# Performance work log

Hardware: AMD Instinct MI355X
Metric: run time of the kernel (lower is better)

The kernel has to match this reference:

```python
import jax, jax.numpy as jnp
import numpy as np

ALPHA = 0.2  # leaky relu slope


def setup_inputs() -> dict:
    key = jax.random.key(0)
    k_h, k_adj, k_w, k_a = jax.random.split(key, 4)
    B, N, F_in, F_out, H = 4, 2048, 128, 64, 4
    h = jax.random.normal(k_h, (B, N, F_in), dtype=jnp.float32)
    adj = jax.random.randint(k_adj, (N, N), 0, 2).astype(jnp.float32)
    # xavier_uniform with gain=1.414 (as in reset_parameters)
    gain = 1.414
    lim_w = gain * np.sqrt(6.0 / (F_in + F_out))
    W = jax.random.uniform(k_w, (H, F_in, F_out), minval=-lim_w, maxval=lim_w, dtype=jnp.float32)
    lim_a = gain * np.sqrt(6.0 / (2 * F_out + 1))
    a = jax.random.uniform(k_a, (H, 2 * F_out, 1), minval=-lim_a, maxval=lim_a, dtype=jnp.float32)
    return {"h": h, "adj": adj, "W": W, "a": a}


def reference(h, adj, W, a):
    B, N, _ = h.shape
    F_out = W.shape[2]
    # per-head linear transform: [B, N, H, F_out]
    ht = jnp.einsum('hio,bni->bnho', W, h)
    # split attention vector into src/dst halves; a^T [h_i; h_j] = a_src.h_i + a_dst.h_j
    a_src = a[:, :F_out, 0]   # [H, F_out]
    a_dst = a[:, F_out:, 0]   # [H, F_out]
    e_src = jnp.einsum('bnho,ho->bnh', ht, a_src)  # score contribution of node i (rows)
    e_dst = jnp.einsum('bnho,ho->bnh', ht, a_dst)  # score contribution of node j (cols)
    e = e_src[:, :, None, :] + e_dst[:, None, :, :]           # [B, N, N, H]
    e = jnp.where(e >= 0, e, ALPHA * e)                        # leaky relu
    e = e + (-1e20 * (1.0 - adj))[None, :, :, None]            # adjacency mask (shared over batch/heads)
    att = jax.nn.softmax(e, axis=2)                            # softmax over neighbors j
    # dropout p=0.0 (eval-mode reference): identity
    h_prime = jnp.einsum('bmnh,bnho->bmho', att, ht)           # [B, N, H, F_out]
    return h_prime.reshape(B, N, -1)                           # concat heads -> [B, N, H*F_out]
```

## Files before the change

kernel.cpp:

```cpp
#include <hip/hip_runtime.h>

#define ALPHA 0.2f
#define LOG2E 1.44269504088896340736f

constexpr int BB  = 4;
constexpr int NN  = 2048;
constexpr int FIN = 128;
constexpr int FO  = 64;
constexpr int HH  = 4;
constexpr int CC  = BB * HH;

using half8   = __attribute__((ext_vector_type(8))) _Float16;
using floatx4 = __attribute__((ext_vector_type(4))) float;

__device__ __forceinline__ float fast_exp2(float x) {
#if __has_builtin(__builtin_amdgcn_exp2f)
  return __builtin_amdgcn_exp2f(x);
#else
  return exp2f(x);
#endif
}

union PK4 { _Float16 f[4]; uint2 u; };

__global__ __launch_bounds__(256) void gat_k1_prep(
    const float* __restrict__ h, const float* __restrict__ W,
    const float* __restrict__ a, _Float16* __restrict__ htT,
    float* __restrict__ esrcT, float* __restrict__ edst) {
  const int blk = blockIdx.x;
  const int c  = blk >> 5;
  const int n0 = (blk & 31) * 64;
  const int b = c >> 2, hh = c & 3;
  const int t = threadIdx.x;
  const int w = t >> 6, lane = t & 63;
  const int q = lane >> 4, r16 = lane & 15;

  __shared__ __align__(16) _Float16 Xs[64 * 128];
  __shared__ __align__(16) _Float16 WT[64 * 128];
  __shared__ float wasb[128];
  __shared__ float wadb[128];

  {
    const int k = t & 127;
    const float* wrow = W + ((size_t)hh * 128 + k) * 64;
    const float* av = a + hh * 128 + ((t >> 7) << 6);
    float s = 0.f;
#pragma unroll
    for (int o = 0; o < 16; ++o) {
      const float4 wv = *(const float4*)(wrow + o * 4);
      const float4 av4 = *(const float4*)(av + o * 4);
      s += wv.x * av4.x + wv.y * av4.y + wv.z * av4.z + wv.w * av4.w;
    }
    if (t < 128) wasb[k] = s; else wadb[k] = s;
  }

  {
    const int k = t >> 1, fh = (t & 1) * 32;
    const float* wsrc = W + ((size_t)hh * 128 + k) * 64 + fh;
    const int chunk = k >> 3, within = k & 7;
#pragma unroll
    for (int i = 0; i < 8; ++i) {
      const float4 v = *(const float4*)(wsrc + i * 4);
      const _Float16 f4[4] = {(_Float16)v.x, (_Float16)v.y,
                              (_Float16)v.z, (_Float16)v.w};
#pragma unroll
      for (int u = 0; u < 4; ++u) {
        const int f = fh + i * 4 + u;
        WT[f * 128 + ((chunk ^ (f & 15)) << 3) + within] = f4[u];
      }
    }
  }

  __syncthreads();

  {
    const int r = t >> 2, cq = t & 3;
    const float* hsrc = h + ((size_t)(b * NN + n0 + r)) * FIN + cq * 32;
    float es = 0.f, ed = 0.f;
#pragma unroll
    for (int i = 0; i < 8; ++i) {
      const float4 v = *(const float4*)(hsrc + i * 4);
      const float4 ws = *(const float4*)&wasb[cq * 32 + i * 4];
      const float4 wd = *(const float4*)&wadb[cq * 32 + i * 4];
      es += v.x * ws.x + v.y * ws.y + v.z * ws.z + v.w * ws.w;
      ed += v.x * wd.x + v.y * wd.y + v.z * wd.z + v.w * wd.w;
      PK4 pk;
      pk.f[0] = (_Float16)v.x; pk.f[1] = (_Float16)v.y;
      pk.f[2] = (_Float16)v.z; pk.f[3] = (_Float16)v.w;
      const int chunk = cq * 4 + (i >> 1);
      *(uint2*)&Xs[r * 128 + ((chunk ^ (r & 15)) << 3) + (i & 1) * 4] = pk.u;
    }
    es += __shfl_xor(es, 1, 64); es += __shfl_xor(es, 2, 64);
    ed += __shfl_xor(ed, 1, 64); ed += __shfl_xor(ed, 2, 64);
    if (cq == 0) {
      esrcT[(size_t)(n0 + r) * CC + c] = es * LOG2E;
      edst[(size_t)c * NN + n0 + r]    = ed * LOG2E;
    }
  }

  __syncthreads();

  floatx4 acc[4];
#pragma unroll
  for (int ft = 0; ft < 4; ++ft) acc[ft] = floatx4{0.f, 0.f, 0.f, 0.f};

  half8 afrag[4];
#pragma unroll
  for (int ks = 0; ks < 4; ++ks) {
    const int slot = (ks * 4 + q) ^ r16;
    afrag[ks] = *(const half8*)&Xs[(w * 16 + r16) * 128 + (slot << 3)];
  }
#pragma unroll
  for (int ks = 0; ks < 4; ++ks) {
#pragma unroll
    for (int ft = 0; ft < 4; ++ft) {
      const int fr = ft * 16 + r16;
      const int slot = (ks * 4 + q) ^ (fr & 15);
      const half8 bfrag = *(const half8*)&WT[fr * 128 + (slot << 3)];
      acc[ft] = __builtin_amdgcn_mfma_f32_16x16x32_f16(afrag[ks], bfrag,
                                                       acc[ft], 0, 0, 0);
    }
  }

#pragma unroll
  for (int ft = 0; ft < 4; ++ft) {
    PK4 pk;
#pragma unroll
    for (int x = 0; x < 4; ++x) pk.f[x] = (_Float16)acc[ft][x];
    const int fcol = ft * 16 + r16;
    const int n = n0 + w * 16 + q * 4;
    *(uint2*)(htT + ((size_t)c * FO + fcol) * NN + n) = pk.u;
  }
}

__global__ __launch_bounds__(256) void gat_k2_stats(
    const float* __restrict__ adj, const float* __restrict__ esrcT,
    const float* __restrict__ edst, unsigned* __restrict__ adjbits,
    float* __restrict__ rmaxT) {
  const int t = threadIdx.x;
  const int w = t >> 6, l = t & 63;
  const int m = blockIdx.x * 4 + w;

  __shared__ float eds[16 * 520];

  float areg[32];
  const float* arow = adj + (size_t)m * NN;
#pragma unroll
  for (int j = 0; j < 32; ++j) areg[j] = arow[j * 64 + l];

#pragma unroll
  for (int j = 0; j < 32; ++j) {
    const unsigned long long mask = __ballot(areg[j] != 0.f);
    if (l == 0) {
      adjbits[m * 64 + j * 2 + 0] = (unsigned)mask;
      adjbits[m * 64 + j * 2 + 1] = (unsigned)(mask >> 32);
    }
  }

  float4 mv[4];
#pragma unroll
  for (int i = 0; i < 4; ++i) mv[i] = float4{-3.0e38f, -3.0e38f, -3.0e38f, -3.0e38f};

  for (int ch = 0; ch < 4; ++ch) {
    __syncthreads();
    {
#pragma unroll
      for (int i = 0; i < 8; ++i) {
        const int idx = t + i * 256;
        const int cc = idx >> 7, nf = idx & 127;
        const float4 v =
            *(const float4*)(edst + (size_t)cc * NN + ch * 512 + nf * 4);
        *(float4*)&eds[cc * 520 + nf * 4] = v;
      }
    }
    __syncthreads();
#pragma unroll
    for (int j2 = 0; j2 < 8; ++j2) {
      const bool on = (areg[ch * 8 + j2] != 0.f);
      const int nl = j2 * 64 + l;
#pragma unroll
      for (int i = 0; i < 4; ++i) {
        float4 e4;
        e4.x = eds[(i * 4 + 0) * 520 + nl];
        e4.y = eds[(i * 4 + 1) * 520 + nl];
        e4.z = eds[(i * 4 + 2) * 520 + nl];
        e4.w = eds[(i * 4 + 3) * 520 + nl];
        mv[i].x = fmaxf(mv[i].x, on ? e4.x : -3.0e38f);
        mv[i].y = fmaxf(mv[i].y, on ? e4.y : -3.0e38f);
        mv[i].z = fmaxf(mv[i].z, on ? e4.z : -3.0e38f);
        mv[i].w = fmaxf(mv[i].w, on ? e4.w : -3.0e38f);
      }
    }
  }

#pragma unroll
  for (int off = 1; off < 64; off <<= 1) {
#pragma unroll
    for (int i = 0; i < 4; ++i) {
      mv[i].x = fmaxf(mv[i].x, __shfl_xor(mv[i].x, off, 64));
      mv[i].y = fmaxf(mv[i].y, __shfl_xor(mv[i].y, off, 64));
      mv[i].z = fmaxf(mv[i].z, __shfl_xor(mv[i].z, off, 64));
      mv[i].w = fmaxf(mv[i].w, __shfl_xor(mv[i].w, off, 64));
    }
  }
  if (l == 0) {
#pragma unroll
    for (int i = 0; i < 4; ++i) {
      const float4 es = *(const float4*)&esrcT[(size_t)m * CC + i * 4];
      float4 o;
      const float sx = es.x + mv[i].x; o.x = (sx >= 0.f) ? sx : ALPHA * sx;
      const float sy = es.y + mv[i].y; o.y = (sy >= 0.f) ? sy : ALPHA * sy;
      const float sz = es.z + mv[i].z; o.z = (sz >= 0.f) ? sz : ALPHA * sz;
      const float sw = es.w + mv[i].w; o.w = (sw >= 0.f) ? sw : ALPHA * sw;
      *(float4*)&rmaxT[(size_t)m * CC + i * 4] = o;
    }
  }
}

__global__ __launch_bounds__(1024) void gat_k3_pv(
    const _Float16* __restrict__ htT, const float* __restrict__ esrcT,
    const float* __restrict__ edst, const unsigned* __restrict__ adjbits,
    const float* __restrict__ rmaxT, float* __restrict__ out) {
  const int blk = blockIdx.x;
  const int c = blk >> 5;
  const int m0 = (blk & 31) * 64;
  const int b = c >> 2, hh = c & 3;
  const int t = threadIdx.x;
  const int w = t >> 6;
  const int kg = w >> 2;
  const int wl = w & 3;
  const int lane = t & 63;
  const int q = lane >> 4, r16 = lane & 15;
  const int row = m0 + wl * 16 + r16;

  __shared__ __align__(16) char smem[64512];
  _Float16* Vt = (_Float16*)smem;
  float* abuf = (float*)smem;

  const float em = esrcT[(size_t)row * CC + c];
  const float rm = rmaxT[(size_t)row * CC + c];
  const float em1 = em - rm;
  const float em2 = fmaf(ALPHA, em, -rm);
  const float* edc = edst + (size_t)c * NN;
  const unsigned* abrow = adjbits + (size_t)row * 64;
  const _Float16* vsrc = htT + (size_t)c * FO * NN;

  const int f0 = t >> 4, sg0 = t & 15;
  const size_t goff0 = (size_t)f0 * NN + (size_t)((sg0 ^ (f0 & 15)) * 8);

  floatx4 acc[4];
#pragma unroll
  for (int ft = 0; ft < 4; ++ft) acc[ft] = floatx4{0.f, 0.f, 0.f, 0.f};
  floatx4 accs = floatx4{0.f, 0.f, 0.f, 0.f};

  half8 ones;
#pragma unroll
  for (int k = 0; k < 8; ++k) ones[k] = (_Float16)1.0f;

#define STAGE(BUF, NBASE)                                                      \
  __builtin_amdgcn_global_load_lds(                                            \
      (const __attribute__((address_space(1))) void*)(vsrc + goff0 + (NBASE)), \
      (__attribute__((address_space(3))) void*)(smem + (BUF)*16384 + t*16),    \
      16, 0, 0)

  STAGE(0, 0);

  for (int step = 0; step < 16; ++step) {
    const int n0k = step * 128 + kg * 32;
    half8 afrag;
    const unsigned bits = abrow[step * 4 + kg] >> (q * 8);
    const float4 ea = *(const float4*)(edc + n0k + q * 8);
    const float4 eb = *(const float4*)(edc + n0k + q * 8 + 4);
    const float xs[8] = {ea.x, ea.y, ea.z, ea.w, eb.x, eb.y, eb.z, eb.w};
#pragma unroll
    for (int k = 0; k < 8; ++k) {
      const float t1 = em1 + xs[k];
      const float t2 = fmaf(ALPHA, xs[k], em2);
      float tt = fmaxf(t1, t2);
      tt = ((bits >> k) & 1u) ? tt : -3.0e38f;
      afrag[k] = (_Float16)fast_exp2(tt);
    }
    __syncthreads();
    if (step + 1 < 16) STAGE((step + 1) & 1, (step + 1) * 128);
    const int bufo = (step & 1) * 8192;
    accs = __builtin_amdgcn_mfma_f32_16x16x32_f16(afrag, ones, accs, 0, 0, 0);
#pragma unroll
    for (int ft = 0; ft < 4; ++ft) {
      const int fr = ft * 16 + r16;
      const int oct = kg * 4 + q;
      const half8 bfrag =
          *(const half8*)&Vt[bufo + fr * 128 + ((oct ^ (fr & 15)) << 3)];
      acc[ft] = __builtin_amdgcn_mfma_f32_16x16x32_f16(afrag, bfrag,
                                                       acc[ft], 0, 0, 0);
    }
  }

  __syncthreads();
  if (kg >= 1) {
    const int base = ((kg - 1) * 256 + (t & 255)) * 21;
#pragma unroll
    for (int ft = 0; ft < 4; ++ft)
#pragma unroll
      for (int x = 0; x < 4; ++x) abuf[base + ft * 4 + x] = acc[ft][x];
#pragma unroll
    for (int x = 0; x < 4; ++x) abuf[base + 16 + x] = accs[x];
  }
  __syncthreads();
  if (kg == 0) {
#pragma unroll
    for (int g = 0; g < 3; ++g) {
      const int base = (g * 256 + t) * 21;
#pragma unroll
      for (int ft = 0; ft < 4; ++ft)
#pragma unroll
        for (int x = 0; x < 4; ++x) acc[ft][x] += abuf[base + ft * 4 + x];
#pragma unroll
      for (int x = 0; x < 4; ++x) accs[x] += abuf[base + 16 + x];
    }
#pragma unroll
    for (int x = 0; x < 4; ++x) {
      const float rinv = 1.0f / accs[x];
      const int mrow = m0 + wl * 16 + q * 4 + x;
      float* op = out + ((size_t)b * NN + mrow) * 256 + hh * 64;
#pragma unroll
      for (int ft = 0; ft < 4; ++ft) op[ft * 16 + r16] = acc[ft][x] * rinv;
    }
  }
#undef STAGE
}

extern "C" void kernel_launch(void* const* d_in, const int* in_sizes, int n_in,
                              void* d_out, int out_size, void* d_ws, size_t ws_size,
                              hipStream_t stream) {
  const float* h   = (const float*)d_in[0];
  const float* adj = (const float*)d_in[1];
  const float* W   = (const float*)d_in[2];
  const float* a   = (const float*)d_in[3];
  float* out = (float*)d_out;

  char* ws = (char*)d_ws;
  _Float16* htT   = (_Float16*)(ws);
  float* esrcT    = (float*)(ws + 4 * 1024 * 1024);
  float* edst     = (float*)(ws + 4 * 1024 * 1024 + 131072);
  unsigned* abits = (unsigned*)(ws + 4 * 1024 * 1024 + 2 * 131072);
  float* rmaxT    = (float*)(ws + 4 * 1024 * 1024 + 2 * 131072 + 524288);

  gat_k1_prep<<<dim3(CC * (NN / 64)), dim3(256), 0, stream>>>(h, W, a, htT, esrcT, edst);
  gat_k2_stats<<<dim3(NN / 4), dim3(256), 0, stream>>>(adj, esrcT, edst, abits, rmaxT);
  gat_k3_pv<<<dim3(CC * (NN / 64)), dim3(1024), 0, stream>>>(htT, esrcT, edst, abits, rmaxT, out);
}
```

Baseline: 128.4 us.

## Replace masked row max with global column max bound and fuse stats kernel

New measurement: 112.1 us. 1.15x faster.

```diff
diff --git a/kernel.cpp b/kernel.cpp
--- a/kernel.cpp
+++ b/kernel.cpp
@@ -23,22 +23,44 @@
 
 union PK4 { _Float16 f[4]; uint2 u; };
 
-__global__ __launch_bounds__(256) void gat_k1_prep(
+__global__ __launch_bounds__(256) void gat_k12(
     const float* __restrict__ h, const float* __restrict__ W,
-    const float* __restrict__ a, _Float16* __restrict__ htT,
-    float* __restrict__ esrcT, float* __restrict__ edst) {
+    const float* __restrict__ a, const float* __restrict__ adj,
+    _Float16* __restrict__ htT, float* __restrict__ esrcT,
+    float* __restrict__ edst, float* __restrict__ gpart,
+    unsigned* __restrict__ adjbits) {
   const int blk = blockIdx.x;
-  const int c  = blk >> 5;
-  const int n0 = (blk & 31) * 64;
-  const int b = c >> 2, hh = c & 3;
   const int t = threadIdx.x;
   const int w = t >> 6, lane = t & 63;
+
+  if (blk >= 512) {
+    const int m = (blk - 512) * 4 + w;
+    float areg[32];
+    const float* arow = adj + (size_t)m * NN;
+#pragma unroll
+    for (int j = 0; j < 32; ++j) areg[j] = arow[j * 64 + lane];
+#pragma unroll
+    for (int j = 0; j < 32; ++j) {
+      const unsigned long long mask = __ballot(areg[j] != 0.f);
+      if (lane == 0) {
+        adjbits[m * 64 + j * 2 + 0] = (unsigned)mask;
+        adjbits[m * 64 + j * 2 + 1] = (unsigned)(mask >> 32);
+      }
+    }
+    return;
+  }
+
+  const int c  = blk >> 5;
+  const int nt = blk & 31;
+  const int n0 = nt * 64;
+  const int b = c >> 2, hh = c & 3;
   const int q = lane >> 4, r16 = lane & 15;
 
   __shared__ __align__(16) _Float16 Xs[64 * 128];
   __shared__ __align__(16) _Float16 WT[64 * 128];
   __shared__ float wasb[128];
   __shared__ float wadb[128];
+  __shared__ float edsh[64];
 
   {
     const int k = t & 127;
@@ -93,12 +115,21 @@
     es += __shfl_xor(es, 1, 64); es += __shfl_xor(es, 2, 64);
     ed += __shfl_xor(ed, 1, 64); ed += __shfl_xor(ed, 2, 64);
     if (cq == 0) {
+      const float edl = ed * LOG2E;
       esrcT[(size_t)(n0 + r) * CC + c] = es * LOG2E;
-      edst[(size_t)c * NN + n0 + r]    = ed * LOG2E;
-    }
-  }
-
-  __syncthreads();
+      edst[(size_t)c * NN + n0 + r]    = edl;
+      edsh[r] = edl;
+    }
+  }
+
+  __syncthreads();
+
+  if (t < 64) {
+    float v = edsh[t];
+#pragma unroll
+    for (int off = 1; off < 64; off <<= 1) v = fmaxf(v, __shfl_xor(v, off, 64));
+    if (t == 0) gpart[c * 32 + nt] = v;
+  }
 
   floatx4 acc[4];
 #pragma unroll
@@ -133,94 +164,10 @@
   }
 }
 
-__global__ __launch_bounds__(256) void gat_k2_stats(
-    const float* __restrict__ adj, const float* __restrict__ esrcT,
-    const float* __restrict__ edst, unsigned* __restrict__ adjbits,
-    float* __restrict__ rmaxT) {
-  const int t = threadIdx.x;
-  const int w = t >> 6, l = t & 63;
-  const int m = blockIdx.x * 4 + w;
-
-  __shared__ float eds[16 * 520];
-
-  float areg[32];
-  const float* arow = adj + (size_t)m * NN;
-#pragma unroll
-  for (int j = 0; j < 32; ++j) areg[j] = arow[j * 64 + l];
-
-#pragma unroll
-  for (int j = 0; j < 32; ++j) {
-    const unsigned long long mask = __ballot(areg[j] != 0.f);
-    if (l == 0) {
-      adjbits[m * 64 + j * 2 + 0] = (unsigned)mask;
-      adjbits[m * 64 + j * 2 + 1] = (unsigned)(mask >> 32);
-    }
-  }
-
-  float4 mv[4];
-#pragma unroll
-  for (int i = 0; i < 4; ++i) mv[i] = float4{-3.0e38f, -3.0e38f, -3.0e38f, -3.0e38f};
-
-  for (int ch = 0; ch < 4; ++ch) {
-    __syncthreads();
-    {
-#pragma unroll
-      for (int i = 0; i < 8; ++i) {
-        const int idx = t + i * 256;
-        const int cc = idx >> 7, nf = idx & 127;
-        const float4 v =
-            *(const float4*)(edst + (size_t)cc * NN + ch * 512 + nf * 4);
-        *(float4*)&eds[cc * 520 + nf * 4] = v;
-      }
-    }
-    __syncthreads();
-#pragma unroll
-    for (int j2 = 0; j2 < 8; ++j2) {
-      const bool on = (areg[ch * 8 + j2] != 0.f);
-      const int nl = j2 * 64 + l;
-#pragma unroll
-      for (int i = 0; i < 4; ++i) {
-        float4 e4;
-        e4.x = eds[(i * 4 + 0) * 520 + nl];
-        e4.y = eds[(i * 4 + 1) * 520 + nl];
-        e4.z = eds[(i * 4 + 2) * 520 + nl];
-        e4.w = eds[(i * 4 + 3) * 520 + nl];
-        mv[i].x = fmaxf(mv[i].x, on ? e4.x : -3.0e38f);
-        mv[i].y = fmaxf(mv[i].y, on ? e4.y : -3.0e38f);
-        mv[i].z = fmaxf(mv[i].z, on ? e4.z : -3.0e38f);
-        mv[i].w = fmaxf(mv[i].w, on ? e4.w : -3.0e38f);
-      }
-    }
-  }
-
-#pragma unroll
-  for (int off = 1; off < 64; off <<= 1) {
-#pragma unroll
-    for (int i = 0; i < 4; ++i) {
-      mv[i].x = fmaxf(mv[i].x, __shfl_xor(mv[i].x, off, 64));
-      mv[i].y = fmaxf(mv[i].y, __shfl_xor(mv[i].y, off, 64));
-      mv[i].z = fmaxf(mv[i].z, __shfl_xor(mv[i].z, off, 64));
-      mv[i].w = fmaxf(mv[i].w, __shfl_xor(mv[i].w, off, 64));
-    }
-  }
-  if (l == 0) {
-#pragma unroll
-    for (int i = 0; i < 4; ++i) {
-      const float4 es = *(const float4*)&esrcT[(size_t)m * CC + i * 4];
-      float4 o;
-      const float sx = es.x + mv[i].x; o.x = (sx >= 0.f) ? sx : ALPHA * sx;
-      const float sy = es.y + mv[i].y; o.y = (sy >= 0.f) ? sy : ALPHA * sy;
-      const float sz = es.z + mv[i].z; o.z = (sz >= 0.f) ? sz : ALPHA * sz;
-      const float sw = es.w + mv[i].w; o.w = (sw >= 0.f) ? sw : ALPHA * sw;
-      *(float4*)&rmaxT[(size_t)m * CC + i * 4] = o;
-    }
-  }
-}
-
 __global__ __launch_bounds__(1024) void gat_k3_pv(
     const _Float16* __restrict__ htT, const float* __restrict__ esrcT,
     const float* __restrict__ edst, const unsigned* __restrict__ adjbits,
-    const float* __restrict__ rmaxT, float* __restrict__ out) {
+    const float* __restrict__ gpart, float* __restrict__ out) {
   const int blk = blockIdx.x;
   const int c = blk >> 5;
   const int m0 = (blk & 31) * 64;
@@ -235,27 +182,15 @@
 
   __shared__ __align__(16) char smem[64512];
   _Float16* Vt = (_Float16*)smem;
+  float* edsF = (float*)(smem + 32768);
+  float* gmaxp = (float*)(smem + 40960);
   float* abuf = (float*)smem;
 
-  const float em = esrcT[(size_t)row * CC + c];
-  const float rm = rmaxT[(size_t)row * CC + c];
-  const float em1 = em - rm;
-  const float em2 = fmaf(ALPHA, em, -rm);
-  const float* edc = edst + (size_t)c * NN;
   const unsigned* abrow = adjbits + (size_t)row * 64;
   const _Float16* vsrc = htT + (size_t)c * FO * NN;
 
   const int f0 = t >> 4, sg0 = t & 15;
   const size_t goff0 = (size_t)f0 * NN + (size_t)((sg0 ^ (f0 & 15)) * 8);
-
-  floatx4 acc[4];
-#pragma unroll
-  for (int ft = 0; ft < 4; ++ft) acc[ft] = floatx4{0.f, 0.f, 0.f, 0.f};
-  floatx4 accs = floatx4{0.f, 0.f, 0.f, 0.f};
-
-  half8 ones;
-#pragma unroll
-  for (int k = 0; k < 8; ++k) ones[k] = (_Float16)1.0f;
 
 #define STAGE(BUF, NBASE)                                                      \
   __builtin_amdgcn_global_load_lds(                                            \
@@ -265,12 +200,40 @@
 
   STAGE(0, 0);
 
+  *(float2*)&edsF[t * 2] = *(const float2*)(edst + (size_t)c * NN + t * 2);
+  {
+    float gv = (t < 32) ? gpart[c * 32 + t] : -3.0e38f;
+    if (t < 64) {
+#pragma unroll
+      for (int off = 1; off < 32; off <<= 1)
+        gv = fmaxf(gv, __shfl_xor(gv, off, 64));
+      if (t == 0) *gmaxp = gv;
+    }
+  }
+  __syncthreads();
+
+  const float em = esrcT[(size_t)row * CC + c];
+  const float gm = *gmaxp;
+  const float s0 = em + gm;
+  const float rm = (s0 >= 0.f) ? s0 : ALPHA * s0;
+  const float em1 = em - rm;
+  const float em2 = fmaf(ALPHA, em, -rm);
+
+  floatx4 acc[4];
+#pragma unroll
+  for (int ft = 0; ft < 4; ++ft) acc[ft] = floatx4{0.f, 0.f, 0.f, 0.f};
+  floatx4 accs = floatx4{0.f, 0.f, 0.f, 0.f};
+
+  half8 ones;
+#pragma unroll
+  for (int k = 0; k < 8; ++k) ones[k] = (_Float16)1.0f;
+
   for (int step = 0; step < 16; ++step) {
     const int n0k = step * 128 + kg * 32;
     half8 afrag;
     const unsigned bits = abrow[step * 4 + kg] >> (q * 8);
-    const float4 ea = *(const float4*)(edc + n0k + q * 8);
-    const float4 eb = *(const float4*)(edc + n0k + q * 8 + 4);
+    const float4 ea = *(const float4*)&edsF[n0k + q * 8];
+    const float4 eb = *(const float4*)&edsF[n0k + q * 8 + 4];
     const float xs[8] = {ea.x, ea.y, ea.z, ea.w, eb.x, eb.y, eb.z, eb.w};
 #pragma unroll
     for (int k = 0; k < 8; ++k) {
@@ -343,9 +306,10 @@
   float* esrcT    = (float*)(ws + 4 * 1024 * 1024);
   float* edst     = (float*)(ws + 4 * 1024 * 1024 + 131072);
   unsigned* abits = (unsigned*)(ws + 4 * 1024 * 1024 + 2 * 131072);
-  float* rmaxT    = (float*)(ws + 4 * 1024 * 1024 + 2 * 131072 + 524288);
-
-  gat_k1_prep<<<dim3(CC * (NN / 64)), dim3(256), 0, stream>>>(h, W, a, htT, esrcT, edst);
-  gat_k2_stats<<<dim3(NN / 4), dim3(256), 0, stream>>>(adj, esrcT, edst, abits, rmaxT);
-  gat_k3_pv<<<dim3(CC * (NN / 64)), dim3(1024), 0, stream>>>(htT, esrcT, edst, abits, rmaxT, out);
+  float* gpart    = (float*)(ws + 4 * 1024 * 1024 + 2 * 131072 + 524288);
+
+  gat_k12<<<dim3(1024), dim3(256), 0, stream>>>(h, W, a, adj, htT, esrcT,
+                                                edst, gpart, abits);
+  gat_k3_pv<<<dim3(CC * (NN / 64)), dim3(1024), 0, stream>>>(htT, esrcT, edst,
+                                                             abits, gpart, out);
 }
```
